# Optimization experiments

Hardware: AMD Instinct MI355X
Metric: run time of the kernel (lower is better)

The kernel has to match this reference:

```python
import jax, jax.numpy as jnp
import numpy as np
import math

B, S, H, NH = 2, 1024, 768, 12
DH = H // NH  # 64

def setup_inputs() -> dict:
    key = jax.random.key(0)
    ks = jax.random.split(key, 8)
    sc = 0.02
    return {
        "hidden_states": jax.random.normal(ks[0], (B, S, H), jnp.float32),
        "bbox_pos_emb": jax.random.normal(ks[1], (S, S, B, DH), jnp.float32),
        "attention_mask": jnp.zeros((B, 1, 1, S), jnp.float32),
        "Wq": jax.random.normal(ks[2], (H, H), jnp.float32) * sc,
        "bq": jnp.zeros((H,), jnp.float32),
        "Wk": jax.random.normal(ks[3], (H, H), jnp.float32) * sc,
        "bk": jnp.zeros((H,), jnp.float32),
        "Wv": jax.random.normal(ks[4], (H, H), jnp.float32) * sc,
        "bv": jnp.zeros((H,), jnp.float32),
    }

def reference(hidden_states, bbox_pos_emb, attention_mask, Wq, bq, Wk, bk, Wv, bv):
    b, s, h = hidden_states.shape
    def proj(W, bias):
        # (b, s, h) -> (b, nh, s, dh)
        y = hidden_states @ W.T + bias
        return y.reshape(b, s, NH, DH).transpose(0, 2, 1, 3)
    q = proj(Wq, bq)
    k = proj(Wk, bk)
    v = proj(Wv, bv)
    # QK^T: (b, nh, s, s)
    scores = jnp.einsum("bnid,bnjd->bnij", q, k)
    # bbox bias: (s, s, b, dh) -> (b, s, s, dh); bnid,bijd->bnij
    bbox = bbox_pos_emb.transpose(2, 0, 1, 3)
    scores = scores + jnp.einsum("bnid,bijd->bnij", q, bbox)
    scores = scores / math.sqrt(DH)
    scores = scores + attention_mask
    probs = jax.nn.softmax(scores, axis=-1)
    ctx = jnp.einsum("bnij,bnjd->bnid", probs, v)
    ctx = ctx.transpose(0, 2, 1, 3).reshape(b, s, h)
    return ctx
```

## Files before the change

### kernel.cpp

```cpp
#include <hip/hip_runtime.h>
#include <hip/hip_bf16.h>

typedef short bf4 __attribute__((ext_vector_type(4)));
typedef short short8 __attribute__((ext_vector_type(8)));
typedef float f32x4 __attribute__((ext_vector_type(4)));

#define MFMA(a, b, c) __builtin_amdgcn_mfma_f32_16x16x32_bf16((a), (b), (c), 0, 0, 0)

#define NB 2
#define NS 1024
#define NHID 768
#define NHEAD 12
#define NDH 64

__device__ __forceinline__ short f2bf(float x) {
    __hip_bfloat16 h = __float2bfloat16(x);
    return *reinterpret_cast<short*>(&h);
}

typedef const __attribute__((address_space(1))) void gas_t;
typedef __attribute__((address_space(3))) void las_t;
__device__ __forceinline__ void gld_lds16(const float* g, float* l) {
    __builtin_amdgcn_global_load_lds((gas_t*)g, (las_t*)l, 16, 0, 0);
}
__device__ __forceinline__ void gld_lds16s(const short* g, short* l) {
    __builtin_amdgcn_global_load_lds((gas_t*)g, (las_t*)l, 16, 0, 0);
}

#define NHE (2048 * 768)
#define WE  (768 * 768)
__global__ void cvt_bf16_all(
    const float* __restrict__ hidden,
    const float* __restrict__ Wq, const float* __restrict__ Wk,
    const float* __restrict__ Wv,
    short* __restrict__ Xbf, short* __restrict__ Wbf)
{
    const int base = (blockIdx.x * 256 + threadIdx.x) * 4;
    const float* src; short* dst; int off;
    if (base < NHE)               { src = hidden; dst = Xbf;          off = base; }
    else if (base < NHE + WE)     { src = Wq;     dst = Wbf;          off = base - NHE; }
    else if (base < NHE + 2 * WE) { src = Wk;     dst = Wbf + WE;     off = base - NHE - WE; }
    else                          { src = Wv;     dst = Wbf + 2 * WE; off = base - NHE - 2 * WE; }
    f32x4 v = *reinterpret_cast<const f32x4*>(src + off);
    bf4 r;
    r[0] = f2bf(v[0]); r[1] = f2bf(v[1]); r[2] = f2bf(v[2]); r[3] = f2bf(v[3]);
    *reinterpret_cast<bf4*>(dst + off) = r;
}

__global__ __launch_bounds__(256, 3) void qkv_gemm(
    const short* __restrict__ Xbf, const short* __restrict__ Wbf,
    const float* __restrict__ bq, const float* __restrict__ bk,
    const float* __restrict__ bv,
    short* __restrict__ Qo, short* __restrict__ Ko, short* __restrict__ VTo)
{
    const int lane = threadIdx.x & 63;
    const int wave = threadIdx.x >> 6;
    const int lg = lane >> 4, lr = lane & 15;

    const int m0 = blockIdx.x * 128;
    const int n0 = blockIdx.y * 64;
    const int proj = n0 / NHID;
    const int ncol0 = n0 % NHID;
    const float* bias = proj == 0 ? bq : (proj == 1 ? bk : bv);

    __shared__ short Alds[2][128 * 64];
    __shared__ short Blds[2][64 * 64];

    f32x4 acc[2][4];
    #pragma unroll
    for (int mm = 0; mm < 2; ++mm)
        #pragma unroll
        for (int s = 0; s < 4; ++s) acc[mm][s] = (f32x4){0.f, 0.f, 0.f, 0.f};

    auto stage = [&](int t, int buf) {
        const int k0 = t * 64;
        #pragma unroll
        for (int p = 0; p < 4; ++p) {
            const int op = wave * 4 + p;
            const int unit = op * 64 + lane;
            const int r = unit >> 3, u = unit & 7;
            const int g = u ^ (r & 7);
            gld_lds16s(Xbf + (size_t)(m0 + r) * NHID + k0 + g * 8,
                       &Alds[buf][op * 512]);
        }
        #pragma unroll
        for (int p = 0; p < 2; ++p) {
            const int op = wave * 2 + p;
            const int unit = op * 64 + lane;
            const int r = unit >> 3, u = unit & 7;
            const int g = u ^ (r & 7);
            gld_lds16s(Wbf + (size_t)(n0 + r) * NHID + k0 + g * 8,
                       &Blds[buf][op * 512]);
        }
    };

    auto compute = [&](int buf) {
        #pragma unroll
        for (int kk = 0; kk < 2; ++kk) {
            const int U = kk * 4 + lg;
            short8 a[2];
            #pragma unroll
            for (int mm = 0; mm < 2; ++mm) {
                const int R = wave * 32 + mm * 16 + lr;
                a[mm] = *reinterpret_cast<const short8*>(
                    &Alds[buf][(R * 8 + (U ^ (R & 7))) * 8]);
            }
            #pragma unroll
            for (int s = 0; s < 4; ++s) {
                const int R = s * 16 + lr;
                short8 b = *reinterpret_cast<const short8*>(
                    &Blds[buf][(R * 8 + (U ^ (R & 7))) * 8]);
                acc[0][s] = MFMA(a[0], b, acc[0][s]);
                acc[1][s] = MFMA(a[1], b, acc[1][s]);
            }
        }
    };

    stage(0, 0);
    #pragma unroll 2
    for (int t = 0; t < 12; ++t) {
        const int buf = t & 1;
        asm volatile("s_waitcnt vmcnt(0)" ::: "memory");
        __syncthreads();
        if (t < 11) stage(t + 1, buf ^ 1);
        compute(buf);
    }

    #pragma unroll
    for (int mm = 0; mm < 2; ++mm) {
        #pragma unroll
        for (int s = 0; s < 4; ++s) {
            const int ncol = ncol0 + s * 16 + lr;
            const float badd = bias[ncol];
            #pragma unroll
            for (int r = 0; r < 4; ++r) {
                const int m = m0 + wave * 32 + mm * 16 + lg * 4 + r;
                const short v16 = f2bf(acc[mm][s][r] + badd);
                if (proj == 0) {
                    Qo[(size_t)m * NHID + ncol] = v16;
                } else if (proj == 1) {
                    Ko[(size_t)m * NHID + ncol] = v16;
                } else {
                    const int b = m >> 10, ss = m & 1023;
                    const int h = ncol >> 6, dd = ncol & 63;
                    VTo[(((size_t)(b * NHEAD + h) * NDH + dd) << 10) + ss] = v16;
                }
            }
        }
    }
}

__global__ __launch_bounds__(256, 2) void bias_gemm(
    const short* __restrict__ Q,
    const float* __restrict__ bbox,
    const float* __restrict__ mask,
    short* __restrict__ biasH)
{
    const int lane = threadIdx.x & 63;
    const int wave = threadIdx.x >> 6;
    const int lg = lane >> 4, lr = lane & 15;
    const int i = blockIdx.x;
    const int jq = wave * 256;

    __shared__ float lds[4][2][2048];

    short8 qa[2][2];
    #pragma unroll
    for (int b2 = 0; b2 < 2; ++b2)
        #pragma unroll
        for (int kk = 0; kk < 2; ++kk)
            qa[b2][kk] = *reinterpret_cast<const short8*>(
                Q + ((size_t)(b2 * NS) + i) * NHID + lr * 64 + kk * 32 + lg * 8);

    const int r_half = lane >> 5;
    const int u_lin = lane & 31;

    auto stage = [&](int t, int buf) {
        const int j0 = jq + t * 16;
        float* dst = &lds[wave][buf][0];
        #pragma unroll
        for (int w = 0; w < 8; ++w) {
            const int r = 2 * w + r_half;
            const int u = u_lin ^ (r & 7);
            const float* src = bbox + (size_t)(i * NS + j0 + r) * 128 + u * 4;
            gld_lds16(src, dst + w * 256);
        }
    };

    auto compute = [&](int t, int buf) {
        const float* tile = &lds[wave][buf][0];
        const int j0 = jq + t * 16;
        const int x = lr & 7;
        #pragma unroll
        for (int b2 = 0; b2 < 2; ++b2) {
            const float mk = mask[b2 * NS + j0 + lr];
            f32x4 c = (f32x4){0.f, 0.f, 0.f, 0.f};
            #pragma unroll
            for (int kk = 0; kk < 2; ++kk) {
                const int q0 = b2 * 16 + kk * 8 + lg * 2;
                f32x4 ca = *reinterpret_cast<const f32x4*>(tile + (size_t)(lr * 32 + ((q0)     ^ x)) * 4);
                f32x4 cb = *reinterpret_cast<const f32x4*>(tile + (size_t)(lr * 32 + ((q0 + 1) ^ x)) * 4);
                short8 bf;
                bf[0] = f2bf(ca[0]); bf[1] = f2bf(ca[1]); bf[2] = f2bf(ca[2]); bf[3] = f2bf(ca[3]);
                bf[4] = f2bf(cb[0]); bf[5] = f2bf(cb[1]); bf[6] = f2bf(cb[2]); bf[7] = f2bf(cb[3]);
                c = MFMA(qa[b2][kk], bf, c);
            }
            if (lg < 3) {
                #pragma unroll
                for (int r = 0; r < 4; ++r) {
                    const int n = lg * 4 + r;
                    biasH[((size_t)(b2 * NHEAD + n) * NS + i) * NS + j0 + lr] =
                        f2bf(c[r] * 0.125f + mk);
                }
            }
        }
    };

    stage(0, 0);
    for (int t = 0; t < 16; ++t) {
        const int buf = t & 1;
        asm volatile("s_waitcnt lgkmcnt(0)" ::: "memory");
        if (t < 15) stage(t + 1, buf ^ 1);
        if (t == 0 || t == 15) asm volatile("s_waitcnt vmcnt(8)"  ::: "memory");
        else                   asm volatile("s_waitcnt vmcnt(16)" ::: "memory");
        compute(t, buf);
    }
}

__global__ __launch_bounds__(256, 3) void attn2(
    const short* __restrict__ Q,
    const short* __restrict__ K,
    const short* __restrict__ VT,
    const short* __restrict__ biasH,
    float* __restrict__ out)
{
    const int lane = threadIdx.x & 63;
    const int wave = threadIdx.x >> 6;
    const int lg = lane >> 4, lr = lane & 15;
    const int i0 = blockIdx.x * 16;
    const int bh = blockIdx.y;
    const int b = bh / NHEAD, h = bh % NHEAD;
    const int jq = wave * 256;

    __shared__ short plds[4][16][40];
    __shared__ short blds[4][2][16 * 40];
    __shared__ float numlds[4][16][68];
    __shared__ float denlds[4][16];

    short8 qa[2];
    #pragma unroll
    for (int kk = 0; kk < 2; ++kk)
        qa[kk] = *reinterpret_cast<const short8*>(
            Q + ((size_t)(b * NS) + i0 + lr) * NHID + h * 64 + kk * 32 + lg * 8);

    const short* Kb = K + (size_t)b * NS * NHID + h * 64;
    const short* Vb = VT + (size_t)(b * NHEAD + h) * NDH * NS;
    const short* Bb = biasH + ((size_t)(b * NHEAD + h) * NS + i0) * NS;

    f32x4 ctx[4];
    #pragma unroll
    for (int dt = 0; dt < 4; ++dt) ctx[dt] = (f32x4){0.f, 0.f, 0.f, 0.f};
    f32x4 den = (f32x4){0.f, 0.f, 0.f, 0.f};

    short8 kfA[4], vfA[4], bvA;
    short8 kfB[4], vfB[4], bvB;

    auto load = [&](int t, short8* kf, short8* vf, short8* bv) {
        const int j0 = jq + t * 32;
        #pragma unroll
        for (int s = 0; s < 2; ++s)
            #pragma unroll
            for (int kk = 0; kk < 2; ++kk)
                kf[s * 2 + kk] = *reinterpret_cast<const short8*>(
                    Kb + (size_t)(j0 + s * 16 + lr) * NHID + kk * 32 + lg * 8);
        #pragma unroll
        for (int dt = 0; dt < 4; ++dt)
            vf[dt] = *reinterpret_cast<const short8*>(
                Vb + (size_t)(dt * 16 + lr) * NS + j0 + lg * 8);
        *bv = *reinterpret_cast<const short8*>(
            Bb + (size_t)(lane >> 2) * NS + j0 + (lane & 3) * 8);
    };

    auto storeB = [&](short8 bv, int buf) {
        *reinterpret_cast<short8*>(
            &blds[wave][buf][(lane >> 2) * 40 + (lane & 3) * 8]) = bv;
        asm volatile("" ::: "memory");
    };

    auto compute = [&](const short8* kf, const short8* vf, int buf) {
        f32x4 sc[2];
        #pragma unroll
        for (int s = 0; s < 2; ++s) {
            f32x4 c = (f32x4){0.f, 0.f, 0.f, 0.f};
            c = MFMA(qa[0], kf[s * 2 + 0], c);
            c = MFMA(qa[1], kf[s * 2 + 1], c);
            sc[s] = c;
        }
        #pragma unroll
        for (int s = 0; s < 2; ++s)
            #pragma unroll
            for (int r = 0; r < 4; ++r) {
                const unsigned int u = (unsigned int)(unsigned short)
                    blds[wave][buf][(lg * 4 + r) * 40 + s * 16 + lr] << 16;
                float bb;
                __builtin_memcpy(&bb, &u, 4);
                sc[s][r] = __expf(sc[s][r] * 0.125f + bb);
            }
        den += sc[0] + sc[1];

        #pragma unroll
        for (int s = 0; s < 2; ++s)
            #pragma unroll
            for (int r = 0; r < 4; ++r)
                plds[wave][lg * 4 + r][s * 16 + lr] = f2bf(sc[s][r]);
        asm volatile("" ::: "memory");
        short8 pa = *reinterpret_cast<const short8*>(&plds[wave][lr][lg * 8]);
        asm volatile("" ::: "memory");

        #pragma unroll
        for (int dt = 0; dt < 4; ++dt) ctx[dt] = MFMA(pa, vf[dt], ctx[dt]);
    };

    load(0, kfA, vfA, &bvA);
    #pragma unroll
    for (int tp = 0; tp < 4; ++tp) {
        const int t = tp * 2;
        storeB(bvA, 0);
        if (t + 1 < 8) load(t + 1, kfB, vfB, &bvB);
        compute(kfA, vfA, 0);
        storeB(bvB, 1);
        if (t + 2 < 8) load(t + 2, kfA, vfA, &bvA);
        compute(kfB, vfB, 1);
    }

    #pragma unroll
    for (int w = 1; w < 16; w <<= 1) {
        f32x4 o;
        #pragma unroll
        for (int r = 0; r < 4; ++r) o[r] = __shfl_xor(den[r], w, 64);
        den += o;
    }

    #pragma unroll
    for (int dt = 0; dt < 4; ++dt)
        #pragma unroll
        for (int r = 0; r < 4; ++r)
            numlds[wave][lg * 4 + r][dt * 16 + lr] = ctx[dt][r];
    if (lr == 0) {
        #pragma unroll
        for (int r = 0; r < 4; ++r) denlds[wave][lg * 4 + r] = den[r];
    }
    __syncthreads();

    const int ti = threadIdx.x >> 4;
    const int tc = (threadIdx.x & 15) * 4;
    f32x4 n = *reinterpret_cast<const f32x4*>(&numlds[0][ti][tc]);
    n += *reinterpret_cast<const f32x4*>(&numlds[1][ti][tc]);
    n += *reinterpret_cast<const f32x4*>(&numlds[2][ti][tc]);
    n += *reinterpret_cast<const f32x4*>(&numlds[3][ti][tc]);
    const float dd = denlds[0][ti] + denlds[1][ti] + denlds[2][ti] + denlds[3][ti];
    const float inv = 1.0f / dd;
    f32x4 o = n * inv;
    *reinterpret_cast<f32x4*>(out + ((size_t)(b * NS) + i0 + ti) * NHID + h * 64 + tc) = o;
}

extern "C" void kernel_launch(void* const* d_in, const int* in_sizes, int n_in,
                              void* d_out, int out_size, void* d_ws, size_t ws_size,
                              hipStream_t stream) {
    (void)in_sizes; (void)n_in; (void)out_size; (void)ws_size;
    const float* hidden = (const float*)d_in[0];
    const float* bbox   = (const float*)d_in[1];
    const float* mask   = (const float*)d_in[2];
    const float* Wq = (const float*)d_in[3]; const float* bq = (const float*)d_in[4];
    const float* Wk = (const float*)d_in[5]; const float* bk = (const float*)d_in[6];
    const float* Wv = (const float*)d_in[7]; const float* bv = (const float*)d_in[8];
    float* out = (float*)d_out;

    char* ws = (char*)d_ws;
    const size_t qkv_bytes = (size_t)NB * NS * NHID * sizeof(short);
    short* Qw  = (short*)ws;
    short* Kw  = (short*)(ws + qkv_bytes);
    short* VTw = (short*)(ws + 2 * qkv_bytes);
    short* biasH = (short*)(ws + 3 * qkv_bytes);
    const size_t bias_bytes = (size_t)NB * NHEAD * NS * NS * sizeof(short);
    short* Xbf = (short*)(ws + 3 * qkv_bytes + bias_bytes);
    short* Wbf = Xbf + (size_t)2048 * NHID;

    const int cvt_total = (NHE + 3 * WE) / 4;
    cvt_bf16_all<<<cvt_total / 256, 256, 0, stream>>>(hidden, Wq, Wk, Wv, Xbf, Wbf);

    dim3 gp(16, 36);
    qkv_gemm<<<gp, 256, 0, stream>>>(Xbf, Wbf, bq, bk, bv, Qw, Kw, VTw);

    bias_gemm<<<NS, 256, 0, stream>>>(Qw, bbox, mask, biasH);

    dim3 ga(NS / 16, NB * NHEAD);
    attn2<<<ga, 256, 0, stream>>>(Qw, Kw, VTw, biasH, out);
}
```

Baseline: 223.0 us.

## Swizzle workgroups across XCDs and deepen bias prefetch in attention

Both the QKV GEMM and the attention kernel now use a flattened 1D grid with an XCD-aware remap. Consecutive logical tiles that share K/V or weight rows land on the same XCD, which should improve L2 reuse. The attention loop is restructured to prefetch the bias tile two iterations ahead in rotating registers, while K/V stay double-buffered. Bias now goes through a single LDS buffer instead of two, which raises register pressure and relies on in-wave ordering for the LDS reuse.

```diff
diff --git a/kernel.cpp b/kernel.cpp
--- a/kernel.cpp
+++ b/kernel.cpp
@@ -16,6 +16,10 @@
 __device__ __forceinline__ short f2bf(float x) {
     __hip_bfloat16 h = __float2bfloat16(x);
     return *reinterpret_cast<short*>(&h);
+}
+
+__device__ __forceinline__ int xcd_swz(int orig, int nwg) {
+    return (orig & 7) * (nwg >> 3) + (orig >> 3);
 }
 
 typedef const __attribute__((address_space(1))) void gas_t;
@@ -57,8 +61,9 @@
     const int wave = threadIdx.x >> 6;
     const int lg = lane >> 4, lr = lane & 15;
 
-    const int m0 = blockIdx.x * 128;
-    const int n0 = blockIdx.y * 64;
+    const int wgid = xcd_swz(blockIdx.x, 16 * 36);
+    const int m0 = (wgid / 36) * 128;
+    const int n0 = (wgid % 36) * 64;
     const int proj = n0 / NHID;
     const int ncol0 = n0 % NHID;
     const float* bias = proj == 0 ? bq : (proj == 1 ? bk : bv);
@@ -237,13 +242,15 @@
     const int lane = threadIdx.x & 63;
     const int wave = threadIdx.x >> 6;
     const int lg = lane >> 4, lr = lane & 15;
-    const int i0 = blockIdx.x * 16;
-    const int bh = blockIdx.y;
+
+    const int wgid = xcd_swz(blockIdx.x, 24 * 64);
+    const int bh = wgid / 64;
+    const int i0 = (wgid % 64) * 16;
     const int b = bh / NHEAD, h = bh % NHEAD;
     const int jq = wave * 256;
 
     __shared__ short plds[4][16][40];
-    __shared__ short blds[4][2][16 * 40];
+    __shared__ short blds[4][16 * 40];
     __shared__ float numlds[4][16][68];
     __shared__ float denlds[4][16];
 
@@ -262,10 +269,11 @@
     for (int dt = 0; dt < 4; ++dt) ctx[dt] = (f32x4){0.f, 0.f, 0.f, 0.f};
     f32x4 den = (f32x4){0.f, 0.f, 0.f, 0.f};
 
-    short8 kfA[4], vfA[4], bvA;
-    short8 kfB[4], vfB[4], bvB;
-
-    auto load = [&](int t, short8* kf, short8* vf, short8* bv) {
+    short8 kfA[4], vfA[4];
+    short8 kfB[4], vfB[4];
+    short8 bv0, bv1, bv2;
+
+    auto kvload = [&](int t, short8* kf, short8* vf) {
         const int j0 = jq + t * 32;
         #pragma unroll
         for (int s = 0; s < 2; ++s)
@@ -277,17 +285,18 @@
         for (int dt = 0; dt < 4; ++dt)
             vf[dt] = *reinterpret_cast<const short8*>(
                 Vb + (size_t)(dt * 16 + lr) * NS + j0 + lg * 8);
-        *bv = *reinterpret_cast<const short8*>(
+    };
+    auto bload = [&](int t) -> short8 {
+        const int j0 = jq + t * 32;
+        return *reinterpret_cast<const short8*>(
             Bb + (size_t)(lane >> 2) * NS + j0 + (lane & 3) * 8);
     };
 
-    auto storeB = [&](short8 bv, int buf) {
+    auto compute = [&](const short8* kf, const short8* vf, short8 bv) {
         *reinterpret_cast<short8*>(
-            &blds[wave][buf][(lane >> 2) * 40 + (lane & 3) * 8]) = bv;
+            &blds[wave][(lane >> 2) * 40 + (lane & 3) * 8]) = bv;
         asm volatile("" ::: "memory");
-    };
-
-    auto compute = [&](const short8* kf, const short8* vf, int buf) {
+
         f32x4 sc[2];
         #pragma unroll
         for (int s = 0; s < 2; ++s) {
@@ -301,7 +310,7 @@
             #pragma unroll
             for (int r = 0; r < 4; ++r) {
                 const unsigned int u = (unsigned int)(unsigned short)
-                    blds[wave][buf][(lg * 4 + r) * 40 + s * 16 + lr] << 16;
+                    blds[wave][(lg * 4 + r) * 40 + s * 16 + lr] << 16;
                 float bb;
                 __builtin_memcpy(&bb, &u, 4);
                 sc[s][r] = __expf(sc[s][r] * 0.125f + bb);
@@ -321,17 +330,17 @@
         for (int dt = 0; dt < 4; ++dt) ctx[dt] = MFMA(pa, vf[dt], ctx[dt]);
     };
 
-    load(0, kfA, vfA, &bvA);
-    #pragma unroll
-    for (int tp = 0; tp < 4; ++tp) {
-        const int t = tp * 2;
-        storeB(bvA, 0);
-        if (t + 1 < 8) load(t + 1, kfB, vfB, &bvB);
-        compute(kfA, vfA, 0);
-        storeB(bvB, 1);
-        if (t + 2 < 8) load(t + 2, kfA, vfA, &bvA);
-        compute(kfB, vfB, 1);
-    }
+    bv0 = bload(0); bv1 = bload(1);
+    kvload(0, kfA, vfA);
+
+    bv2 = bload(2); kvload(1, kfB, vfB); compute(kfA, vfA, bv0);
+    bv0 = bload(3); kvload(2, kfA, vfA); compute(kfB, vfB, bv1);
+    bv1 = bload(4); kvload(3, kfB, vfB); compute(kfA, vfA, bv2);
+    bv2 = bload(5); kvload(4, kfA, vfA); compute(kfB, vfB, bv0);
+    bv0 = bload(6); kvload(5, kfB, vfB); compute(kfA, vfA, bv1);
+    bv1 = bload(7); kvload(6, kfA, vfA); compute(kfB, vfB, bv2);
+    kvload(7, kfB, vfB);                 compute(kfA, vfA, bv0);
+    compute(kfB, vfB, bv1);
 
     #pragma unroll
     for (int w = 1; w < 16; w <<= 1) {
@@ -389,11 +398,9 @@
     const int cvt_total = (NHE + 3 * WE) / 4;
     cvt_bf16_all<<<cvt_total / 256, 256, 0, stream>>>(hidden, Wq, Wk, Wv, Xbf, Wbf);
 
-    dim3 gp(16, 36);
-    qkv_gemm<<<gp, 256, 0, stream>>>(Xbf, Wbf, bq, bk, bv, Qw, Kw, VTw);
+    qkv_gemm<<<16 * 36, 256, 0, stream>>>(Xbf, Wbf, bq, bk, bv, Qw, Kw, VTw);
 
     bias_gemm<<<NS, 256, 0, stream>>>(Qw, bbox, mask, biasH);
 
-    dim3 ga(NS / 16, NB * NHEAD);
-    attn2<<<ga, 256, 0, stream>>>(Qw, Kw, VTw, biasH, out);
-}
+    attn2<<<24 * 64, 256, 0, stream>>>(Qw, Kw, VTw, biasH, out);
+}
```

After: 225.2 us. No clear change (+1.0%).
